# Optimization experiments

Measured on AMD Instinct MI355X. Metric: run time of the kernel, lower is better.

The kernel has to match this reference:

```python
import jax, jax.numpy as jnp
import numpy as np

EPS = 1e-5


def setup_inputs() -> dict:
    key = jax.random.key(0)
    k1, k2, k3, k4 = jax.random.split(key, 4)
    B, C, H, W = 4, 64, 128, 256
    Hg, Wg = 512, 1024
    NC = 19  # num_class; loop also covers ignore label 255 -> NC+1 entries
    x = jax.random.normal(k1, (B, C, H, W), dtype=jnp.float32)
    gt = jax.random.randint(k2, (B, Hg, Wg), 0, 19).astype(jnp.int32)
    eps_mu = jax.random.normal(k3, (NC + 1, B, C), dtype=jnp.float32)
    eps_std = jax.random.normal(k4, (NC + 1, B, C), dtype=jnp.float32)
    return {"x": x, "gt": gt, "eps_mu": eps_mu, "eps_std": eps_std}


def _sqrtvar(t):
    # torch .var(dim=0) is unbiased (ddof=1); repeat over batch is just broadcast
    return jnp.sqrt(jnp.var(t, axis=0, ddof=1, keepdims=True) + EPS)


def reference(x, gt, eps_mu, eps_std):
    B, C, H, W = x.shape
    NC1 = eps_mu.shape[0]  # num_class + 1 (ignore label 255)
    Hg, Wg = gt.shape[1], gt.shape[2]
    # nearest resize of the (binary) mask == compare on nearest-resized labels
    # torch F.interpolate nearest: src = floor(dst * in/out)
    ih = (jnp.arange(H) * Hg) // H
    iw = (jnp.arange(W) * Wg) // W
    gt_r = gt[:, ih[:, None], iw[None, :]]  # [B,H,W]
    class_ids = jnp.concatenate(
        [jnp.arange(NC1 - 1), jnp.array([255])]).astype(gt.dtype)

    def per_class(carry, inp):
        cid, emu, estd = inp
        mask = (gt_r == cid).astype(x.dtype)[:, None]  # [B,1,H,W]
        mx = x * mask
        npx = jnp.sum(mask, axis=(2, 3))               # [B,1]
        npx = jnp.where(npx == 0, jnp.ones_like(npx), npx)
        mean = jnp.sum(mx, axis=(2, 3)) / npx          # [B,C] == mean*wh/npx
        var = jnp.sum((mask * (mx - mean[:, :, None, None])) ** 2,
                      axis=(2, 3)) / npx
        std = jnp.sqrt(var + EPS)                      # [B,C]
        beta = mean + emu * _sqrtvar(mean)
        gamma = std + estd * _sqrtvar(std)
        xn = (mx - mean[:, :, None, None]) / std[:, :, None, None]
        out = mask * (xn * gamma[:, :, None, None] + beta[:, :, None, None])
        return carry + out, None

    class_x, _ = jax.lax.scan(per_class, jnp.zeros_like(x),
                              (class_ids, eps_mu, eps_std))
    return class_x
```

## Files before the change

kernel.cpp:

```cpp
#include <hip/hip_runtime.h>

#define EPS 1e-5f
constexpr int B = 4, C = 64, H = 128, W = 256;
constexpr int Hg = 512, Wg = 1024;
constexpr int NC = 19;
constexpr int HW = H * W;
constexpr int HW4 = HW / 4;

__global__ __launch_bounds__(256) void k_pack(const int* __restrict__ gt,
                                              unsigned int* __restrict__ gt_p) {
  int t = threadIdx.x;
  int R = blockIdx.x * 4 + (t >> 6);
  int ws = t & 63;
  int b = R >> 7, h = R & 127;
  const int* row = gt + (size_t)(b * Hg + h * 4) * Wg;
  unsigned int c0 = (unsigned int)row[(ws * 4 + 0) * 4];
  unsigned int c1 = (unsigned int)row[(ws * 4 + 1) * 4];
  unsigned int c2 = (unsigned int)row[(ws * 4 + 2) * 4];
  unsigned int c3 = (unsigned int)row[(ws * 4 + 3) * 4];
  gt_p[R * 64 + ws] = c0 | (c1 << 8) | (c2 << 16) | (c3 << 24);
}

__global__ __launch_bounds__(256) void k_stats(const float* __restrict__ x,
                                               const unsigned int* __restrict__ gt_p,
                                               float* __restrict__ sums_p,
                                               float* __restrict__ sqs_p,
                                               int* __restrict__ counts_p) {
  __shared__ float2 acc[NC * 256];
  __shared__ int hist[NC];
  int t = threadIdx.x;
  for (int k = t; k < NC * 256; k += 256) acc[k] = make_float2(0.f, 0.f);
  int plane = blockIdx.x >> 2;
  int q = blockIdx.x & 3;
  int b = plane >> 6, c = plane & 63;
  bool desig = (c == 0);
  if (desig && t < NC) hist[t] = 0;
  __syncthreads();

  const float4* xp = (const float4*)x + (size_t)plane * (HW / 4) + q * 2048;
  const unsigned int* gp = gt_p + (size_t)b * HW4 + q * 2048;
  for (int j = 0; j < 8; j++) {
    int i = j * 256 + t;
    float4 v = xp[i];
    unsigned int g = gp[i];
    int c0 = g & 255, c1 = (g >> 8) & 255, c2 = (g >> 16) & 255, c3 = g >> 24;
    float2 a;
    a = acc[c0 * 256 + t]; a.x += v.x; a.y += v.x * v.x; acc[c0 * 256 + t] = a;
    a = acc[c1 * 256 + t]; a.x += v.y; a.y += v.y * v.y; acc[c1 * 256 + t] = a;
    a = acc[c2 * 256 + t]; a.x += v.z; a.y += v.z * v.z; acc[c2 * 256 + t] = a;
    a = acc[c3 * 256 + t]; a.x += v.w; a.y += v.w * v.w; acc[c3 * 256 + t] = a;
    if (desig) {
      atomicAdd(&hist[c0], 1); atomicAdd(&hist[c1], 1);
      atomicAdd(&hist[c2], 1); atomicAdd(&hist[c3], 1);
    }
  }
  __syncthreads();

  int w = t >> 6, lane = t & 63;
  for (int k = w; k < NC; k += 4) {
    float2 a0 = acc[k * 256 + lane];
    float2 a1 = acc[k * 256 + 64 + lane];
    float2 a2 = acc[k * 256 + 128 + lane];
    float2 a3 = acc[k * 256 + 192 + lane];
    float s  = a0.x + a1.x + a2.x + a3.x;
    float qq = a0.y + a1.y + a2.y + a3.y;
    for (int m = 32; m >= 1; m >>= 1) {
      s  += __shfl_xor(s, m, 64);
      qq += __shfl_xor(qq, m, 64);
    }
    if (lane == 0) {
      int e = (k * B + b) * C + c;
      sums_p[e * 4 + q] = s;
      sqs_p [e * 4 + q] = qq;
    }
  }
  if (desig && t < NC) counts_p[(b * NC + t) * 4 + q] = hist[t];
}

__global__ __launch_bounds__(256) void k_apply(const float* __restrict__ x,
                                               const unsigned int* __restrict__ gt_p,
                                               const float* __restrict__ sums_p,
                                               const float* __restrict__ sqs_p,
                                               const int* __restrict__ counts_p,
                                               const float* __restrict__ eps_mu,
                                               const float* __restrict__ eps_std,
                                               float* __restrict__ out) {
  __shared__ float2 tab[NC];
  int t = threadIdx.x;
  int plane = blockIdx.x >> 2;
  int q = blockIdx.x & 3;
  int b = plane >> 6, c = plane & 63;
  const float4* xp = (const float4*)x + (size_t)plane * (HW / 4) + q * 2048;
  const unsigned int* gp = gt_p + (size_t)b * HW4 + q * 2048;
  float4* op = (float4*)out + (size_t)plane * (HW / 4) + q * 2048;

  float4 v0 = xp[t];
  unsigned int g0 = gp[t];

  if (t < NC) {
    float mean[B], stdv[B];
    float msum = 0.f, ssum = 0.f;
    for (int bb = 0; bb < B; bb++) {
      int4 cn = *(const int4*)&counts_p[(bb * NC + t) * 4];
      float n = (float)(cn.x + cn.y + cn.z + cn.w);
      if (n == 0.f) n = 1.f;
      float4 s4 = *(const float4*)&sums_p[((t * B + bb) * C + c) * 4];
      float4 q4 = *(const float4*)&sqs_p [((t * B + bb) * C + c) * 4];
      float s  = s4.x + s4.y + s4.z + s4.w;
      float qq = q4.x + q4.y + q4.z + q4.w;
      float m = s / n;
      float var = qq / n - m * m;
      var = var > 0.f ? var : 0.f;
      mean[bb] = m;
      stdv[bb] = sqrtf(var + EPS);
      msum += m; ssum += stdv[bb];
    }
    float mbar = msum * 0.25f, sbar = ssum * 0.25f;
    float vm = 0.f, vs = 0.f;
    for (int bb = 0; bb < B; bb++) {
      float dm = mean[bb] - mbar; vm += dm * dm;
      float ds = stdv[bb] - sbar; vs += ds * ds;
    }
    float sqvm = sqrtf(vm * (1.f / 3.f) + EPS);
    float sqvs = sqrtf(vs * (1.f / 3.f) + EPS);
    int e = (t * B + b) * C + c;
    float beta  = mean[b] + eps_mu[e]  * sqvm;
    float gamma = stdv[b] + eps_std[e] * sqvs;
    float sc = gamma / stdv[b];
    tab[t] = make_float2(sc, beta - mean[b] * sc);
  }
  __syncthreads();

  {
    float2 a0 = tab[g0 & 255], a1 = tab[(g0 >> 8) & 255];
    float2 a2 = tab[(g0 >> 16) & 255], a3 = tab[g0 >> 24];
    float4 o;
    o.x = fmaf(v0.x, a0.x, a0.y);
    o.y = fmaf(v0.y, a1.x, a1.y);
    o.z = fmaf(v0.z, a2.x, a2.y);
    o.w = fmaf(v0.w, a3.x, a3.y);
    op[t] = o;
  }
  for (int j = 1; j < 8; j++) {
    int i = j * 256 + t;
    float4 v = xp[i];
    unsigned int g = gp[i];
    float2 a0 = tab[g & 255], a1 = tab[(g >> 8) & 255];
    float2 a2 = tab[(g >> 16) & 255], a3 = tab[g >> 24];
    float4 o;
    o.x = fmaf(v.x, a0.x, a0.y);
    o.y = fmaf(v.y, a1.x, a1.y);
    o.z = fmaf(v.z, a2.x, a2.y);
    o.w = fmaf(v.w, a3.x, a3.y);
    op[i] = o;
  }
}

extern "C" void kernel_launch(void* const* d_in, const int* in_sizes, int n_in,
                              void* d_out, int out_size, void* d_ws, size_t ws_size,
                              hipStream_t stream) {
  const float* x       = (const float*)d_in[0];
  const int*   gt      = (const int*)  d_in[1];
  const float* eps_mu  = (const float*)d_in[2];
  const float* eps_std = (const float*)d_in[3];
  float* out = (float*)d_out;

  char* ws = (char*)d_ws;
  unsigned int* gt_p    = (unsigned int*)(ws);
  float*        sums_p  = (float*)(ws + 131072);
  float*        sqs_p   = (float*)(ws + 208896);
  int*          counts_p= (int*)  (ws + 286720);

  hipLaunchKernelGGL(k_pack,  dim3(B * H / 4), dim3(256), 0, stream, gt, gt_p);
  hipLaunchKernelGGL(k_stats, dim3(B * C * 4), dim3(256), 0, stream,
                     x, gt_p, sums_p, sqs_p, counts_p);
  hipLaunchKernelGGL(k_apply, dim3(B * C * 4), dim3(256), 0, stream,
                     x, gt_p, sums_p, sqs_p, counts_p, eps_mu, eps_std, out);
}
```

Measured before the change: 105.6 us.

## Shrink stats LDS with per-lane atomics, move class histogram to pack, split planes 8-way

The stats kernel replaces its 38 KB per-thread float2 LDS accumulator with two small per-lane arrays updated by LDS float atomics, which cuts shared memory so more blocks can fit per CU. Each plane is now split into 8 blocks instead of 4, and partial sums are written 8 per entry. The class pixel histogram moves from the c==0 stats blocks into the pack kernel, which writes per-block counts that the apply kernel sums. The trade-off is LDS atomic contention when the four waves that share a lane index hit the same class, plus more partials to reduce.

```diff
diff --git a/kernel.cpp b/kernel.cpp
--- a/kernel.cpp
+++ b/kernel.cpp
@@ -8,8 +8,12 @@
 constexpr int HW4 = HW / 4;
 
 __global__ __launch_bounds__(256) void k_pack(const int* __restrict__ gt,
-                                              unsigned int* __restrict__ gt_p) {
+                                              unsigned int* __restrict__ gt_p,
+                                              int* __restrict__ counts_pb) {
+  __shared__ int hist[NC];
   int t = threadIdx.x;
+  if (t < NC) hist[t] = 0;
+  __syncthreads();
   int R = blockIdx.x * 4 + (t >> 6);
   int ws = t & 63;
   int b = R >> 7, h = R & 127;
@@ -19,69 +23,61 @@
   unsigned int c2 = (unsigned int)row[(ws * 4 + 2) * 4];
   unsigned int c3 = (unsigned int)row[(ws * 4 + 3) * 4];
   gt_p[R * 64 + ws] = c0 | (c1 << 8) | (c2 << 16) | (c3 << 24);
+  atomicAdd(&hist[c0], 1); atomicAdd(&hist[c1], 1);
+  atomicAdd(&hist[c2], 1); atomicAdd(&hist[c3], 1);
+  __syncthreads();
+  if (t < NC) counts_pb[t * 128 + blockIdx.x] = hist[t];
 }
 
 __global__ __launch_bounds__(256) void k_stats(const float* __restrict__ x,
                                                const unsigned int* __restrict__ gt_p,
                                                float* __restrict__ sums_p,
-                                               float* __restrict__ sqs_p,
-                                               int* __restrict__ counts_p) {
-  __shared__ float2 acc[NC * 256];
-  __shared__ int hist[NC];
+                                               float* __restrict__ sqs_p) {
+  __shared__ float accS[NC * 64];
+  __shared__ float accQ[NC * 64];
   int t = threadIdx.x;
-  for (int k = t; k < NC * 256; k += 256) acc[k] = make_float2(0.f, 0.f);
-  int plane = blockIdx.x >> 2;
-  int q = blockIdx.x & 3;
+  for (int k = t; k < NC * 64; k += 256) { accS[k] = 0.f; accQ[k] = 0.f; }
+  __syncthreads();
+  int plane = blockIdx.x >> 3;
+  int e8 = blockIdx.x & 7;
   int b = plane >> 6, c = plane & 63;
-  bool desig = (c == 0);
-  if (desig && t < NC) hist[t] = 0;
-  __syncthreads();
+  int lane = t & 63;
 
-  const float4* xp = (const float4*)x + (size_t)plane * (HW / 4) + q * 2048;
-  const unsigned int* gp = gt_p + (size_t)b * HW4 + q * 2048;
-  for (int j = 0; j < 8; j++) {
+  const float4* xp = (const float4*)x + (size_t)plane * (HW / 4) + e8 * 1024;
+  const unsigned int* gp = gt_p + (size_t)b * HW4 + e8 * 1024;
+  for (int j = 0; j < 4; j++) {
     int i = j * 256 + t;
     float4 v = xp[i];
     unsigned int g = gp[i];
     int c0 = g & 255, c1 = (g >> 8) & 255, c2 = (g >> 16) & 255, c3 = g >> 24;
-    float2 a;
-    a = acc[c0 * 256 + t]; a.x += v.x; a.y += v.x * v.x; acc[c0 * 256 + t] = a;
-    a = acc[c1 * 256 + t]; a.x += v.y; a.y += v.y * v.y; acc[c1 * 256 + t] = a;
-    a = acc[c2 * 256 + t]; a.x += v.z; a.y += v.z * v.z; acc[c2 * 256 + t] = a;
-    a = acc[c3 * 256 + t]; a.x += v.w; a.y += v.w * v.w; acc[c3 * 256 + t] = a;
-    if (desig) {
-      atomicAdd(&hist[c0], 1); atomicAdd(&hist[c1], 1);
-      atomicAdd(&hist[c2], 1); atomicAdd(&hist[c3], 1);
-    }
+    atomicAdd(&accS[c0 * 64 + lane], v.x); atomicAdd(&accQ[c0 * 64 + lane], v.x * v.x);
+    atomicAdd(&accS[c1 * 64 + lane], v.y); atomicAdd(&accQ[c1 * 64 + lane], v.y * v.y);
+    atomicAdd(&accS[c2 * 64 + lane], v.z); atomicAdd(&accQ[c2 * 64 + lane], v.z * v.z);
+    atomicAdd(&accS[c3 * 64 + lane], v.w); atomicAdd(&accQ[c3 * 64 + lane], v.w * v.w);
   }
   __syncthreads();
 
-  int w = t >> 6, lane = t & 63;
+  int w = t >> 6;
   for (int k = w; k < NC; k += 4) {
-    float2 a0 = acc[k * 256 + lane];
-    float2 a1 = acc[k * 256 + 64 + lane];
-    float2 a2 = acc[k * 256 + 128 + lane];
-    float2 a3 = acc[k * 256 + 192 + lane];
-    float s  = a0.x + a1.x + a2.x + a3.x;
-    float qq = a0.y + a1.y + a2.y + a3.y;
+    float s  = accS[k * 64 + lane];
+    float qq = accQ[k * 64 + lane];
     for (int m = 32; m >= 1; m >>= 1) {
       s  += __shfl_xor(s, m, 64);
       qq += __shfl_xor(qq, m, 64);
     }
     if (lane == 0) {
       int e = (k * B + b) * C + c;
-      sums_p[e * 4 + q] = s;
-      sqs_p [e * 4 + q] = qq;
+      sums_p[e * 8 + e8] = s;
+      sqs_p [e * 8 + e8] = qq;
     }
   }
-  if (desig && t < NC) counts_p[(b * NC + t) * 4 + q] = hist[t];
 }
 
 __global__ __launch_bounds__(256) void k_apply(const float* __restrict__ x,
                                                const unsigned int* __restrict__ gt_p,
                                                const float* __restrict__ sums_p,
                                                const float* __restrict__ sqs_p,
-                                               const int* __restrict__ counts_p,
+                                               const int* __restrict__ counts_pb,
                                                const float* __restrict__ eps_mu,
                                                const float* __restrict__ eps_std,
                                                float* __restrict__ out) {
@@ -101,13 +97,17 @@
     float mean[B], stdv[B];
     float msum = 0.f, ssum = 0.f;
     for (int bb = 0; bb < B; bb++) {
-      int4 cn = *(const int4*)&counts_p[(bb * NC + t) * 4];
-      float n = (float)(cn.x + cn.y + cn.z + cn.w);
-      if (n == 0.f) n = 1.f;
-      float4 s4 = *(const float4*)&sums_p[((t * B + bb) * C + c) * 4];
-      float4 q4 = *(const float4*)&sqs_p [((t * B + bb) * C + c) * 4];
-      float s  = s4.x + s4.y + s4.z + s4.w;
-      float qq = q4.x + q4.y + q4.z + q4.w;
+      const int4* cp = (const int4*)&counts_pb[t * 128 + bb * 32];
+      int isum = 0;
+      for (int j = 0; j < 8; j++) { int4 cv = cp[j]; isum += cv.x + cv.y + cv.z + cv.w; }
+      float n = isum > 0 ? (float)isum : 1.f;
+      int e = (t * B + bb) * C + c;
+      float4 sa = *(const float4*)&sums_p[e * 8];
+      float4 sb = *(const float4*)&sums_p[e * 8 + 4];
+      float4 qa = *(const float4*)&sqs_p [e * 8];
+      float4 qb = *(const float4*)&sqs_p [e * 8 + 4];
+      float s  = (sa.x + sa.y + sa.z + sa.w) + (sb.x + sb.y + sb.z + sb.w);
+      float qq = (qa.x + qa.y + qa.z + qa.w) + (qb.x + qb.y + qb.z + qb.w);
       float m = s / n;
       float var = qq / n - m * m;
       var = var > 0.f ? var : 0.f;
@@ -166,14 +166,14 @@
   float* out = (float*)d_out;
 
   char* ws = (char*)d_ws;
-  unsigned int* gt_p    = (unsigned int*)(ws);
-  float*        sums_p  = (float*)(ws + 131072);
-  float*        sqs_p   = (float*)(ws + 208896);
-  int*          counts_p= (int*)  (ws + 286720);
+  unsigned int* gt_p     = (unsigned int*)(ws);
+  float*        sums_p   = (float*)(ws + 131072);
+  float*        sqs_p    = (float*)(ws + 286720);
+  int*          counts_pb= (int*)  (ws + 442368);
 
-  hipLaunchKernelGGL(k_pack,  dim3(B * H / 4), dim3(256), 0, stream, gt, gt_p);
-  hipLaunchKernelGGL(k_stats, dim3(B * C * 4), dim3(256), 0, stream,
-                     x, gt_p, sums_p, sqs_p, counts_p);
+  hipLaunchKernelGGL(k_pack,  dim3(B * H / 4), dim3(256), 0, stream, gt, gt_p, counts_pb);
+  hipLaunchKernelGGL(k_stats, dim3(B * C * 8), dim3(256), 0, stream,
+                     x, gt_p, sums_p, sqs_p);
   hipLaunchKernelGGL(k_apply, dim3(B * C * 4), dim3(256), 0, stream,
-                     x, gt_p, sums_p, sqs_p, counts_p, eps_mu, eps_std, out);
+                     x, gt_p, sums_p, sqs_p, counts_pb, eps_mu, eps_std, out);
 }
```

Result: slower. 186.4 us (+76.6%).
